# Optimization experiments

Measured on AMD Instinct MI355X. Metric: run time of the kernel, lower is better.

## Reference

```python
import jax, jax.numpy as jnp
import numpy as np

DELTA = 2.0

def _pearson(x, y):
    vx = x - jnp.mean(x)
    vy = y - jnp.mean(y)
    return jnp.sum(vx * vy) / (jnp.sqrt(jnp.sum(vx ** 2)) * jnp.sqrt(jnp.sum(vy ** 2)))

def setup_inputs() -> dict:
    key = jax.random.key(0)
    k1, k2 = jax.random.split(key)
    n = 4000000
    output = jax.random.normal(k1, (n, 6), dtype=jnp.float32)
    label = jax.random.normal(k2, (n, 1), dtype=jnp.float32)
    return {"output": output, "label": label}

def reference(output, label):
    # output: [n, 6] = [q0, q1, q2, q3, q4, q]; label: [n, 1]
    target = label[:, 0]  # [n]

    # Pearson correlation of each of the 6 prediction columns vs label
    plcc = [_pearson(output[:, i], target) for i in range(6)]

    # Per-sample weighted pseudo-Huber loss (vectorized over batch)
    diff = output - label                      # [n, 6] (pred - target)
    huber = DELTA ** 2 * (jnp.sqrt(1.0 + (diff / DELTA) ** 2) - 1.0)  # [n, 6]
    alpha_head = 0.2 * jnp.tanh(diff[:, :5]) ** 2                     # [n, 5]
    alpha = jnp.concatenate([alpha_head, jnp.ones_like(diff[:, 5:6])], axis=1)  # [n, 6]
    loss_old = jnp.mean(jnp.sum(huber * alpha, axis=1))

    p0, p1, p2, p3, p4, p5 = plcc
    s = 5.0 - p0 - p1 - p2 - p3 - p4
    plcc_pen = ((1 - p0) ** 2 + (1 - p1) ** 2 + (1 - p2) ** 2 + (1 - p3) ** 2 + (1 - p4) ** 2) / s
    loss = loss_old + plcc_pen + (1.0 - p5)
    return loss
```

## Files before the change

### kernel.cpp

```cpp
#include <hip/hip_runtime.h>
#include <math.h>

static constexpr int BLOCK     = 256;
static constexpr int NACC      = 21;
static constexpr int PSTRIDE   = 24;
static constexpr int TILE_ROWS = 512;
static constexpr int TILE_F4   = TILE_ROWS * 6 / 4;
static constexpr int MAXBLOCKS = 2048;

__device__ __forceinline__ float fast_tanh_sq(float d) {
    float e = __expf(2.0f * d);
    float r = __builtin_amdgcn_rcpf(e + 1.0f);
    float t = 1.0f - 2.0f * r;
    return t * t;
}

__device__ __forceinline__ void row_accum(float acc[NACC], const float x[6], float y) {
    acc[18] += y;
    acc[19] += y * y;
    float rowh = 0.0f;
#pragma unroll
    for (int c = 0; c < 6; ++c) {
        const float xv = x[c];
        acc[c]      += xv;
        acc[6 + c]  += xv * xv;
        acc[12 + c] += xv * y;
        const float d   = xv - y;
        const float hub = 4.0f * (__builtin_amdgcn_sqrtf(1.0f + 0.25f * d * d) - 1.0f);
        const float al  = (c < 5) ? (0.2f * fast_tanh_sq(d)) : 1.0f;
        rowh += hub * al;
    }
    acc[20] += rowh;
}

__global__ __launch_bounds__(BLOCK) void huber_partial_kernel(
    const float* __restrict__ out6,
    const float* __restrict__ lab,
    float* __restrict__ part,
    int n)
{
    __shared__ float4 tile[TILE_F4];
    __shared__ float  red[BLOCK / 64][NACC];

    float acc[NACC];
#pragma unroll
    for (int k = 0; k < NACC; ++k) acc[k] = 0.0f;

    const int t  = threadIdx.x;
    const int n2 = n & ~1;
    const long long nf4 = ((long long)n2 * 6) >> 2;
    const int ntiles = (n2 + TILE_ROWS - 1) / TILE_ROWS;
    const float4* gsrc = reinterpret_cast<const float4*>(out6);

    for (int tl = blockIdx.x; tl < ntiles; tl += gridDim.x) {
        const long long basef4 = (long long)tl * TILE_F4;

#pragma unroll
        for (int k = 0; k < 3; ++k) {
            const long long g = basef4 + k * BLOCK + t;
            float4 v = make_float4(0.f, 0.f, 0.f, 0.f);
            if (g < nf4) v = gsrc[g];
            tile[k * BLOCK + t] = v;
        }

        const int r0 = tl * TILE_ROWS + 2 * t;
        float2 y2 = make_float2(0.f, 0.f);
        if (r0 + 1 < n2)
            y2 = *reinterpret_cast<const float2*>(lab + r0);
        __syncthreads();

        if (r0 + 1 < n2) {
            const float4 a = tile[3 * t + 0];
            const float4 b = tile[3 * t + 1];
            const float4 c = tile[3 * t + 2];
            const float r0v[6] = {a.x, a.y, a.z, a.w, b.x, b.y};
            const float r1v[6] = {b.z, b.w, c.x, c.y, c.z, c.w};
            row_accum(acc, r0v, y2.x);
            row_accum(acc, r1v, y2.y);
        }
        __syncthreads();
    }

    if ((n & 1) && blockIdx.x == 0 && t == 0) {
        const size_t row = (size_t)n - 1;
        float xr[6];
#pragma unroll
        for (int c = 0; c < 6; ++c) xr[c] = out6[row * 6 + c];
        row_accum(acc, xr, lab[row]);
    }

#pragma unroll
    for (int k = 0; k < NACC; ++k) {
        float v = acc[k];
#pragma unroll
        for (int off = 32; off > 0; off >>= 1)
            v += __shfl_down(v, off, 64);
        acc[k] = v;
    }

    const int wave = t >> 6;
    const int lane = t & 63;
    if (lane == 0) {
#pragma unroll
        for (int k = 0; k < NACC; ++k) red[wave][k] = acc[k];
    }
    __syncthreads();
    if (t < NACC) {
        float s = 0.0f;
#pragma unroll
        for (int w = 0; w < BLOCK / 64; ++w) s += red[w][t];
        part[(size_t)blockIdx.x * PSTRIDE + t] = s;
    }
}

__global__ __launch_bounds__(BLOCK) void huber_final_kernel(
    const float* __restrict__ part, int nblocks, int n, float* __restrict__ out)
{
    __shared__ double sred[BLOCK / 64][NACC];

    double acc[NACC];
#pragma unroll
    for (int k = 0; k < NACC; ++k) acc[k] = 0.0;

    for (int b = threadIdx.x; b < nblocks; b += BLOCK) {
        const float* p = part + (size_t)b * PSTRIDE;
        const float4* p4 = reinterpret_cast<const float4*>(p);
#pragma unroll
        for (int q = 0; q < 5; ++q) {
            const float4 v = p4[q];
            acc[q * 4 + 0] += (double)v.x;
            acc[q * 4 + 1] += (double)v.y;
            acc[q * 4 + 2] += (double)v.z;
            acc[q * 4 + 3] += (double)v.w;
        }
        acc[20] += (double)p[20];
    }

#pragma unroll
    for (int k = 0; k < NACC; ++k) {
        double v = acc[k];
#pragma unroll
        for (int off = 32; off > 0; off >>= 1)
            v += __shfl_down(v, off, 64);
        acc[k] = v;
    }

    const int wave = threadIdx.x >> 6;
    const int lane = threadIdx.x & 63;
    if (lane == 0) {
#pragma unroll
        for (int k = 0; k < NACC; ++k) sred[wave][k] = acc[k];
    }
    __syncthreads();

    if (threadIdx.x == 0) {
        double tot[NACC];
#pragma unroll
        for (int k = 0; k < NACC; ++k) {
            double s = 0.0;
#pragma unroll
            for (int w = 0; w < BLOCK / 64; ++w) s += sred[w][k];
            tot[k] = s;
        }

        const double dn  = (double)n;
        const double Sy  = tot[18];
        const double Syy = tot[19];
        const double vary = Syy - Sy * Sy / dn;
        double pc[6];
#pragma unroll
        for (int c = 0; c < 6; ++c) {
            const double Sx  = tot[c];
            const double Sxx = tot[6 + c];
            const double Sxy = tot[12 + c];
            const double cov  = Sxy - Sx * Sy / dn;
            const double varx = Sxx - Sx * Sx / dn;
            pc[c] = cov / (sqrt(varx) * sqrt(vary));
        }
        const double loss_old = tot[20] / dn;
        const double s = 5.0 - pc[0] - pc[1] - pc[2] - pc[3] - pc[4];
        double pen = 0.0;
#pragma unroll
        for (int c = 0; c < 5; ++c) pen += (1.0 - pc[c]) * (1.0 - pc[c]);
        pen /= s;
        const double loss = loss_old + pen + (1.0 - pc[5]);
        out[0] = (float)loss;
    }
}

extern "C" void kernel_launch(void* const* d_in, const int* in_sizes, int n_in,
                              void* d_out, int out_size, void* d_ws, size_t ws_size,
                              hipStream_t stream) {
    const float* out6 = (const float*)d_in[0];
    const float* lab  = (const float*)d_in[1];
    float* out = (float*)d_out;
    const int n = in_sizes[1];

    const int n2 = n & ~1;
    int ntiles = (n2 + TILE_ROWS - 1) / TILE_ROWS;
    if (ntiles < 1) ntiles = 1;

    int nblocks = MAXBLOCKS;
    const int maxb = (int)(ws_size / (PSTRIDE * sizeof(float)));
    if (nblocks > maxb)   nblocks = maxb;
    if (nblocks > ntiles) nblocks = ntiles;
    if (nblocks < 1)      nblocks = 1;

    float* part = (float*)d_ws;
    hipLaunchKernelGGL(huber_partial_kernel, dim3(nblocks), dim3(BLOCK), 0, stream,
                       out6, lab, part, n);
    hipLaunchKernelGGL(huber_final_kernel, dim3(1), dim3(BLOCK), 0, stream,
                       part, nblocks, n, out);
}
```

Baseline: 165.5 us.

## Load tiles straight into LDS with global_load_lds and double tile size

Replaces the register-staged global-to-shared copy with direct global-to-LDS async loads, and doubles the tile to 1024 rows so each thread handles two row pairs per iteration. Full tiles run without bounds checks, and block 0 handles the remainder rows with direct global reads. This is meant to cut VGPR traffic and per-tile loop overhead. The risks are that __syncthreads may not wait correctly for the async LDS writes (vmcnt), that LDS use doubles, and that fewer tiles per block leaves less parallelism.

```diff
diff --git a/kernel.cpp b/kernel.cpp
--- a/kernel.cpp
+++ b/kernel.cpp
@@ -4,9 +4,16 @@
 static constexpr int BLOCK     = 256;
 static constexpr int NACC      = 21;
 static constexpr int PSTRIDE   = 24;
-static constexpr int TILE_ROWS = 512;
+static constexpr int TILE_ROWS = 1024;
 static constexpr int TILE_F4   = TILE_ROWS * 6 / 4;
 static constexpr int MAXBLOCKS = 2048;
+
+__device__ __forceinline__ void async_f4(const float4* g, float4* l) {
+    __builtin_amdgcn_global_load_lds(
+        (const __attribute__((address_space(1))) void*)g,
+        (__attribute__((address_space(3))) void*)l,
+        16, 0, 0);
+}
 
 __device__ __forceinline__ float fast_tanh_sq(float d) {
     float e = __expf(2.0f * d);
@@ -33,6 +40,15 @@
     acc[20] += rowh;
 }
 
+__device__ __forceinline__ void chunk_accum(float acc[NACC],
+                                            const float4 a, const float4 b,
+                                            const float4 c, const float2 y2) {
+    const float r0v[6] = {a.x, a.y, a.z, a.w, b.x, b.y};
+    const float r1v[6] = {b.z, b.w, c.x, c.y, c.z, c.w};
+    row_accum(acc, r0v, y2.x);
+    row_accum(acc, r1v, y2.y);
+}
+
 __global__ __launch_bounds__(BLOCK) void huber_partial_kernel(
     const float* __restrict__ out6,
     const float* __restrict__ lab,
@@ -48,45 +64,45 @@
 
     const int t  = threadIdx.x;
     const int n2 = n & ~1;
-    const long long nf4 = ((long long)n2 * 6) >> 2;
-    const int ntiles = (n2 + TILE_ROWS - 1) / TILE_ROWS;
+    const int full_tiles = n2 / TILE_ROWS;
+    const int tail_start = full_tiles * TILE_ROWS;
+
     const float4* gsrc = reinterpret_cast<const float4*>(out6);
-
-    for (int tl = blockIdx.x; tl < ntiles; tl += gridDim.x) {
+    const float2* lab2 = reinterpret_cast<const float2*>(lab);
+
+    for (int tl = blockIdx.x; tl < full_tiles; tl += gridDim.x) {
         const long long basef4 = (long long)tl * TILE_F4;
 
 #pragma unroll
-        for (int k = 0; k < 3; ++k) {
-            const long long g = basef4 + k * BLOCK + t;
-            float4 v = make_float4(0.f, 0.f, 0.f, 0.f);
-            if (g < nf4) v = gsrc[g];
-            tile[k * BLOCK + t] = v;
-        }
-
-        const int r0 = tl * TILE_ROWS + 2 * t;
-        float2 y2 = make_float2(0.f, 0.f);
-        if (r0 + 1 < n2)
-            y2 = *reinterpret_cast<const float2*>(lab + r0);
+        for (int k = 0; k < 6; ++k)
+            async_f4(&gsrc[basef4 + k * BLOCK + t], &tile[k * BLOCK + t]);
+
+        const float2 yA = lab2[(size_t)tl * (TILE_ROWS / 2) + t];
+        const float2 yB = lab2[(size_t)tl * (TILE_ROWS / 2) + BLOCK + t];
+
         __syncthreads();
 
-        if (r0 + 1 < n2) {
-            const float4 a = tile[3 * t + 0];
-            const float4 b = tile[3 * t + 1];
-            const float4 c = tile[3 * t + 2];
-            const float r0v[6] = {a.x, a.y, a.z, a.w, b.x, b.y};
-            const float r1v[6] = {b.z, b.w, c.x, c.y, c.z, c.w};
-            row_accum(acc, r0v, y2.x);
-            row_accum(acc, r1v, y2.y);
-        }
+        chunk_accum(acc, tile[3 * t + 0], tile[3 * t + 1], tile[3 * t + 2], yA);
+        chunk_accum(acc, tile[TILE_F4 / 2 + 3 * t + 0],
+                         tile[TILE_F4 / 2 + 3 * t + 1],
+                         tile[TILE_F4 / 2 + 3 * t + 2], yB);
+
         __syncthreads();
     }
 
-    if ((n & 1) && blockIdx.x == 0 && t == 0) {
-        const size_t row = (size_t)n - 1;
-        float xr[6];
-#pragma unroll
-        for (int c = 0; c < 6; ++c) xr[c] = out6[row * 6 + c];
-        row_accum(acc, xr, lab[row]);
+    if (blockIdx.x == 0) {
+        for (int r = tail_start + 2 * t; r + 1 < n2 + 1; r += 2 * BLOCK) {
+            if (r + 1 >= n2) break;
+            const long long g = (long long)r * 3 / 2;
+            chunk_accum(acc, gsrc[g], gsrc[g + 1], gsrc[g + 2], lab2[r >> 1]);
+        }
+        if ((n & 1) && t == 0) {
+            const size_t row = (size_t)n - 1;
+            float xr[6];
+#pragma unroll
+            for (int c = 0; c < 6; ++c) xr[c] = out6[row * 6 + c];
+            row_accum(acc, xr, lab[row]);
+        }
     }
 
 #pragma unroll
@@ -197,14 +213,14 @@
     const int n = in_sizes[1];
 
     const int n2 = n & ~1;
-    int ntiles = (n2 + TILE_ROWS - 1) / TILE_ROWS;
-    if (ntiles < 1) ntiles = 1;
+    int full_tiles = n2 / TILE_ROWS;
+    if (full_tiles < 1) full_tiles = 1;
 
     int nblocks = MAXBLOCKS;
     const int maxb = (int)(ws_size / (PSTRIDE * sizeof(float)));
-    if (nblocks > maxb)   nblocks = maxb;
-    if (nblocks > ntiles) nblocks = ntiles;
-    if (nblocks < 1)      nblocks = 1;
+    if (nblocks > maxb)       nblocks = maxb;
+    if (nblocks > full_tiles) nblocks = full_tiles;
+    if (nblocks < 1)          nblocks = 1;
 
     float* part = (float*)d_ws;
     hipLaunchKernelGGL(huber_partial_kernel, dim3(nblocks), dim3(BLOCK), 0, stream,
```

Result: no change. 163.0 us (-1.5%).
